# Kernel tuning notes

Measured on AMD Instinct MI355X. Metric: run time of the kernel, lower is better.

## Reference

```python
import jax, jax.numpy as jnp
import numpy as np

B, D, H, S = 65536, 256, 4, 64
HD = D // H  # head_dim = 64
EPS = 1e-8


def _lin(x, W, b):
    # torch nn.Linear: y = x @ W.T + b, W: [out, in]
    return x @ W.T + b


def _cos_attn(q_heads, keys, vals):
    # q_heads: [B,H,hd]; keys/vals: [H,S,hd] (shared across batch)
    qn = q_heads / (jnp.linalg.norm(q_heads, axis=-1, keepdims=True) + EPS)
    kn = keys / (jnp.linalg.norm(keys, axis=-1, keepdims=True) + EPS)
    sim = jnp.einsum('bhd,hsd->bhs', qn, kn)          # cosine sims, temp=1.0
    attn = jax.nn.softmax(sim, axis=-1)
    return jnp.einsum('bhs,hsd->bhd', attn, vals)     # [B,H,hd]


def setup_inputs() -> dict:
    key = jax.random.key(0)
    ks = jax.random.split(key, 20)

    def xavier(k, shape):
        fan_in, fan_out = shape[1], shape[0]
        lim = np.sqrt(6.0 / (fan_in + fan_out))
        return jax.random.uniform(k, shape, jnp.float32, -lim, lim)

    return {
        'query': jax.random.normal(ks[0], (B, D), jnp.float32),
        'context': jax.random.normal(ks[1], (B, D), jnp.float32),
        'fast_keys': 0.01 * jax.random.normal(ks[2], (H, S, HD), jnp.float32),
        'fast_vals': 0.01 * jax.random.normal(ks[3], (H, S, HD), jnp.float32),
        'deep_keys': 0.01 * jax.random.normal(ks[4], (H, S, HD), jnp.float32),
        'deep_vals': 0.01 * jax.random.normal(ks[5], (H, S, HD), jnp.float32),
        'Wq': xavier(ks[6], (D, D)), 'bq': jnp.zeros((D,), jnp.float32),
        'Wg': xavier(ks[7], (D, D)), 'bg': jnp.zeros((D,), jnp.float32),
        'Wc1': xavier(ks[8], (D // 2, D)), 'bc1': jnp.zeros((D // 2,), jnp.float32),
        'Wc2': xavier(ks[9], (1, D // 2)), 'bc2': jnp.zeros((1,), jnp.float32),
        'Wo': xavier(ks[10], (D, D)), 'bo': jnp.zeros((D,), jnp.float32),
        'Ws': xavier(ks[11], (D, D)), 'bs': jnp.zeros((D,), jnp.float32),
        'mix_logit': jnp.zeros((), jnp.float32),
        'surprise_mean': jnp.zeros((1, D), jnp.float32),
        'surprise_var': jnp.ones((1, D), jnp.float32),
    }


def reference(query, context, fast_keys, fast_vals, deep_keys, deep_vals,
              Wq, bq, Wg, bg, Wc1, bc1, Wc2, bc2, Wo, bo, Ws, bs,
              mix_logit, surprise_mean, surprise_var):
    # --- query projection and head split ---
    q = _lin(query, Wq, bq)                       # [B, D]
    q_heads = q.reshape(B, H, HD)                 # [B, H, hd]

    # --- dual-tier cosine-similarity attention reads ---
    v_fast = _cos_attn(q_heads, fast_keys, fast_vals).reshape(B, D)
    v_deep = _cos_attn(q_heads, deep_keys, deep_vals).reshape(B, D)

    # --- context-gated mixing of tiers ---
    gate = jnp.tanh(_lin(context, Wg, bg)).mean(axis=-1, keepdims=True)  # [B,1]
    mix = jax.nn.sigmoid(mix_logit + gate)
    out = mix * v_fast + (1.0 - mix) * v_deep

    # --- adaptive retrieval confidence head ---
    conf = jax.nn.sigmoid(_lin(jnp.tanh(_lin(context, Wc1, bc1)), Wc2, bc2))  # [B,1]
    out = out * conf
    out = _lin(out, Wo, bo)                       # [B, d_value]

    # --- surprise (detached diagnostic, does not feed output) ---
    h = jax.lax.stop_gradient(_lin(context, Ws, bs))
    z = (h - surprise_mean) / jnp.sqrt(surprise_var + 1e-6)
    surprise = jax.nn.sigmoid(jnp.abs(z).mean(axis=-1) - 2.0)  # 1/max(0.5,0.1)=2.0
    del surprise  # aux diagnostic; main output is the retrieved vector
    return out
```

## Files before the change

kernel.cpp:

```cpp
#include <hip/hip_runtime.h>

typedef unsigned short u16;
typedef __attribute__((ext_vector_type(8))) short bf16x8;
typedef __attribute__((ext_vector_type(4))) float f32x4;
typedef __attribute__((ext_vector_type(4))) unsigned short u16x4;

#define MFMA16(a, b, c) __builtin_amdgcn_mfma_f32_16x16x32_bf16((a), (b), (c), 0, 0, 0)

#define OFF_WQ   0
#define OFF_WG   65536
#define OFF_WC1  131072
#define OFF_WO   163840
#define OFF_KNF  229376
#define OFF_VTF  245760
#define OFF_KND  262144
#define OFF_VTD  278528

__device__ __forceinline__ u16 f2b(float f) {
  union { float f; unsigned u; } v; v.f = f;
  unsigned r = v.u + 0x7fffu + ((v.u >> 16) & 1u);
  return (u16)(r >> 16);
}
__device__ __forceinline__ float fsig(float x) {
  return __builtin_amdgcn_rcpf(1.f + __expf(-x));
}
__device__ __forceinline__ float ftanh(float x) {
  float e = __expf(2.f * x);
  return (e - 1.f) * __builtin_amdgcn_rcpf(e + 1.f);
}
__device__ __forceinline__ float sum16(float v) {
  v += __shfl_xor(v, 1);
  v += __shfl_xor(v, 2);
  v += __shfl_xor(v, 4);
  v += __shfl_xor(v, 8);
  return v;
}

__global__ void k_convert(const float* __restrict__ Wq, const float* __restrict__ Wg,
                          const float* __restrict__ Wc1, const float* __restrict__ Wo,
                          u16* __restrict__ ws) {
  int i = blockIdx.x * 256 + threadIdx.x;
  ws[OFF_WQ + i] = f2b(Wq[i]);
  ws[OFF_WG + i] = f2b(Wg[i]);
  ws[OFF_WO + i] = f2b(Wo[i]);
  if (i < 32768) ws[OFF_WC1 + i] = f2b(Wc1[i]);
}

__global__ void k_prep(const float* __restrict__ fk, const float* __restrict__ fv,
                       const float* __restrict__ dk, const float* __restrict__ dv,
                       u16* __restrict__ ws) {
  int t = blockIdx.x * 64 + threadIdx.x;
  int h = t >> 6, s = t & 63;
  const float* p;
  float ss, sc;

  p = fk + t * 64; ss = 0.f;
  for (int d = 0; d < 64; ++d) { float x = p[d]; ss += x * x; }
  sc = __builtin_amdgcn_rcpf(__builtin_amdgcn_sqrtf(ss) + 1e-8f);
  for (int d = 0; d < 64; ++d) ws[OFF_KNF + t * 64 + d] = f2b(p[d] * sc);

  p = dk + t * 64; ss = 0.f;
  for (int d = 0; d < 64; ++d) { float x = p[d]; ss += x * x; }
  sc = __builtin_amdgcn_rcpf(__builtin_amdgcn_sqrtf(ss) + 1e-8f);
  for (int d = 0; d < 64; ++d) ws[OFF_KND + t * 64 + d] = f2b(p[d] * sc);

  p = fv + t * 64;
  for (int d = 0; d < 64; ++d) ws[OFF_VTF + h * 4096 + d * 64 + s] = f2b(p[d]);
  p = dv + t * 64;
  for (int d = 0; d < 64; ++d) ws[OFF_VTD + h * 4096 + d * 64 + s] = f2b(p[d]);
}

__global__ __launch_bounds__(256, 2)
void k_fused(const float* __restrict__ query, const float* __restrict__ context,
             const float* __restrict__ bq, const float* __restrict__ bg,
             const float* __restrict__ bc1, const float* __restrict__ Wc2,
             const float* __restrict__ bc2v, const float* __restrict__ bo,
             const float* __restrict__ mixl, const u16* __restrict__ ws,
             float* __restrict__ outp) {
  __shared__ u16 sX[64 * 256];
  __shared__ float red_g[4][64];
  __shared__ float red_c[4][64];
  __shared__ float sA[64];
  __shared__ float sB[64];

  const int t = threadIdx.x;
  const int w = t >> 6;
  const int lane = t & 63;
  const int quad = lane >> 4;
  const int l16 = lane & 15;
  const int row4 = quad * 4;
  const int blk = blockIdx.x;
  char* Xb = (char*)sX;
  char* chunk = Xb + w * 8192;

  auto stage = [&](const float* src) {
    #pragma unroll
    for (int i = 0; i < 16; ++i) {
      int e = i * 1024 + t * 4;
      float4 v = *(const float4*)(src + e);
      int row = e >> 8, col = e & 255;
      u16x4 pk;
      pk.x = f2b(v.x); pk.y = f2b(v.y); pk.z = f2b(v.z); pk.w = f2b(v.w);
      *(u16x4*)(Xb + row * 512 + ((((col >> 3) ^ (row & 7)) << 4) | ((col & 7) << 1))) = pk;
    }
  };
  auto ldA = [&](int row, int kb) {
    return *(const bf16x8*)(Xb + row * 512 + ((((kb >> 3) ^ (row & 7)) << 4)));
  };
  auto ldC = [&](int row, int kb) {
    return *(const bf16x8*)(chunk + row * 128 + ((((kb >> 3) ^ (row & 7)) << 4)));
  };
  auto cwr = [&](int row, int col, u16 v) {
    *(u16*)(chunk + row * 128 + (((((col >> 3) ^ (row & 7)) << 3) | (col & 7)) << 1)) = v;
  };

  const f32x4 vzero = {0.f, 0.f, 0.f, 0.f};

  stage(context + (size_t)blk * 16384);
  __syncthreads();

  {
    f32x4 acc[4][4];
    #pragma unroll
    for (int mt = 0; mt < 4; ++mt)
      #pragma unroll
      for (int nt = 0; nt < 4; ++nt) acc[mt][nt] = vzero;
    const u16* WB = ws + OFF_WG + (w * 64 + l16) * 256;
    #pragma unroll
    for (int kk = 0; kk < 8; ++kk) {
      int kb = kk * 32 + quad * 8;
      bf16x8 a0 = ldA(l16, kb), a1 = ldA(16 + l16, kb), a2 = ldA(32 + l16, kb), a3 = ldA(48 + l16, kb);
      #pragma unroll
      for (int nt = 0; nt < 4; ++nt) {
        bf16x8 b = *(const bf16x8*)(WB + nt * 4096 + kb);
        acc[0][nt] = MFMA16(a0, b, acc[0][nt]);
        acc[1][nt] = MFMA16(a1, b, acc[1][nt]);
        acc[2][nt] = MFMA16(a2, b, acc[2][nt]);
        acc[3][nt] = MFMA16(a3, b, acc[3][nt]);
      }
    }
    float bgv[4];
    #pragma unroll
    for (int nt = 0; nt < 4; ++nt) bgv[nt] = bg[w * 64 + nt * 16 + l16];
    #pragma unroll
    for (int mt = 0; mt < 4; ++mt)
      #pragma unroll
      for (int r = 0; r < 4; ++r) {
        float s = 0.f;
        #pragma unroll
        for (int nt = 0; nt < 4; ++nt) s += ftanh(acc[mt][nt][r] + bgv[nt]);
        s = sum16(s);
        if (l16 == 0) red_g[w][mt * 16 + row4 + r] = s;
      }
  }
  {
    f32x4 acc[4][2];
    #pragma unroll
    for (int mt = 0; mt < 4; ++mt) { acc[mt][0] = vzero; acc[mt][1] = vzero; }
    const u16* WB = ws + OFF_WC1 + (w * 32 + l16) * 256;
    #pragma unroll
    for (int kk = 0; kk < 8; ++kk) {
      int kb = kk * 32 + quad * 8;
      bf16x8 a0 = ldA(l16, kb), a1 = ldA(16 + l16, kb), a2 = ldA(32 + l16, kb), a3 = ldA(48 + l16, kb);
      #pragma unroll
      for (int nt = 0; nt < 2; ++nt) {
        bf16x8 b = *(const bf16x8*)(WB + nt * 4096 + kb);
        acc[0][nt] = MFMA16(a0, b, acc[0][nt]);
        acc[1][nt] = MFMA16(a1, b, acc[1][nt]);
        acc[2][nt] = MFMA16(a2, b, acc[2][nt]);
        acc[3][nt] = MFMA16(a3, b, acc[3][nt]);
      }
    }
    float bcv[2], wcv[2];
    #pragma unroll
    for (int nt = 0; nt < 2; ++nt) {
      int n = w * 32 + nt * 16 + l16;
      bcv[nt] = bc1[n]; wcv[nt] = Wc2[n];
    }
    #pragma unroll
    for (int mt = 0; mt < 4; ++mt)
      #pragma unroll
      for (int r = 0; r < 4; ++r) {
        float s = 0.f;
        #pragma unroll
        for (int nt = 0; nt < 2; ++nt) s += ftanh(acc[mt][nt][r] + bcv[nt]) * wcv[nt];
        s = sum16(s);
        if (l16 == 0) red_c[w][mt * 16 + row4 + r] = s;
      }
  }
  __syncthreads();
  if (t < 64) {
    float g = (red_g[0][t] + red_g[1][t] + red_g[2][t] + red_g[3][t]) * (1.f / 256.f);
    float mix = fsig(mixl[0] + g);
    float conf = fsig(red_c[0][t] + red_c[1][t] + red_c[2][t] + red_c[3][t] + bc2v[0]);
    sA[t] = conf * mix;
    sB[t] = conf - conf * mix;
  }
  __syncthreads();

  stage(query + (size_t)blk * 16384);
  __syncthreads();

  f32x4 qa[4][4];
  {
    #pragma unroll
    for (int mt = 0; mt < 4; ++mt)
      #pragma unroll
      for (int nt = 0; nt < 4; ++nt) qa[mt][nt] = vzero;
    const u16* WB = ws + OFF_WQ + (w * 64 + l16) * 256;
    #pragma unroll
    for (int kk = 0; kk < 8; ++kk) {
      int kb = kk * 32 + quad * 8;
      bf16x8 a0 = ldA(l16, kb), a1 = ldA(16 + l16, kb), a2 = ldA(32 + l16, kb), a3 = ldA(48 + l16, kb);
      #pragma unroll
      for (int nt = 0; nt < 4; ++nt) {
        bf16x8 b = *(const bf16x8*)(WB + nt * 4096 + kb);
        qa[0][nt] = MFMA16(a0, b, qa[0][nt]);
        qa[1][nt] = MFMA16(a1, b, qa[1][nt]);
        qa[2][nt] = MFMA16(a2, b, qa[2][nt]);
        qa[3][nt] = MFMA16(a3, b, qa[3][nt]);
      }
    }
    float bqv[4];
    #pragma unroll
    for (int nt = 0; nt < 4; ++nt) bqv[nt] = bq[w * 64 + nt * 16 + l16];
    #pragma unroll
    for (int mt = 0; mt < 4; ++mt)
      #pragma unroll
      for (int nt = 0; nt < 4; ++nt)
        #pragma unroll
        for (int r = 0; r < 4; ++r) qa[mt][nt][r] += bqv[nt];
  }
  float scl[4][4];
  #pragma unroll
  for (int mt = 0; mt < 4; ++mt)
    #pragma unroll
    for (int r = 0; r < 4; ++r) {
      float ss = 0.f;
      #pragma unroll
      for (int nt = 0; nt < 4; ++nt) ss += qa[mt][nt][r] * qa[mt][nt][r];
      ss = sum16(ss);
      scl[mt][r] = __builtin_amdgcn_rcpf(__builtin_amdgcn_sqrtf(ss) + 1e-8f);
    }
  __syncthreads();

  #pragma unroll
  for (int mt = 0; mt < 4; ++mt)
    #pragma unroll
    for (int r = 0; r < 4; ++r) {
      int row = mt * 16 + row4 + r;
      #pragma unroll
      for (int nt = 0; nt < 4; ++nt)
        cwr(row, nt * 16 + l16, f2b(qa[mt][nt][r] * scl[mt][r]));
    }

  f32x4 sf[4][4], sd[4][4];
  #pragma unroll
  for (int mt = 0; mt < 4; ++mt)
    #pragma unroll
    for (int nt = 0; nt < 4; ++nt) { sf[mt][nt] = vzero; sd[mt][nt] = vzero; }
  {
    const u16* knF = ws + OFF_KNF + w * 4096;
    const u16* knD = ws + OFF_KND + w * 4096;
    #pragma unroll
    for (int kk = 0; kk < 2; ++kk) {
      int kb = kk * 32 + quad * 8;
      bf16x8 a0 = ldC(l16, kb), a1 = ldC(16 + l16, kb), a2 = ldC(32 + l16, kb), a3 = ldC(48 + l16, kb);
      #pragma unroll
      for (int nt = 0; nt < 4; ++nt) {
        bf16x8 bF = *(const bf16x8*)(knF + (nt * 16 + l16) * 64 + kb);
        bf16x8 bD = *(const bf16x8*)(knD + (nt * 16 + l16) * 64 + kb);
        sf[0][nt] = MFMA16(a0, bF, sf[0][nt]);
        sf[1][nt] = MFMA16(a1, bF, sf[1][nt]);
        sf[2][nt] = MFMA16(a2, bF, sf[2][nt]);
        sf[3][nt] = MFMA16(a3, bF, sf[3][nt]);
        sd[0][nt] = MFMA16(a0, bD, sd[0][nt]);
        sd[1][nt] = MFMA16(a1, bD, sd[1][nt]);
        sd[2][nt] = MFMA16(a2, bD, sd[2][nt]);
        sd[3][nt] = MFMA16(a3, bD, sd[3][nt]);
      }
    }
  }

  f32x4 oacc[4][4];
  {
    #pragma unroll
    for (int mt = 0; mt < 4; ++mt)
      #pragma unroll
      for (int r = 0; r < 4; ++r) {
        float rs = 0.f;
        #pragma unroll
        for (int nt = 0; nt < 4; ++nt) { float e = __expf(sf[mt][nt][r]); sf[mt][nt][r] = e; rs += e; }
        rs = sum16(rs);
        float inv = __builtin_amdgcn_rcpf(rs);
        int row = mt * 16 + row4 + r;
        #pragma unroll
        for (int nt = 0; nt < 4; ++nt) cwr(row, nt * 16 + l16, f2b(sf[mt][nt][r] * inv));
      }
    f32x4 pv[4][4];
    #pragma unroll
    for (int mt = 0; mt < 4; ++mt)
      #pragma unroll
      for (int nt = 0; nt < 4; ++nt) pv[mt][nt] = vzero;
    const u16* vT = ws + OFF_VTF + w * 4096;
    #pragma unroll
    for (int kk = 0; kk < 2; ++kk) {
      int kb = kk * 32 + quad * 8;
      bf16x8 a0 = ldC(l16, kb), a1 = ldC(16 + l16, kb), a2 = ldC(32 + l16, kb), a3 = ldC(48 + l16, kb);
      #pragma unroll
      for (int nt = 0; nt < 4; ++nt) {
        bf16x8 b = *(const bf16x8*)(vT + (nt * 16 + l16) * 64 + kb);
        pv[0][nt] = MFMA16(a0, b, pv[0][nt]);
        pv[1][nt] = MFMA16(a1, b, pv[1][nt]);
        pv[2][nt] = MFMA16(a2, b, pv[2][nt]);
        pv[3][nt] = MFMA16(a3, b, pv[3][nt]);
      }
    }
    #pragma unroll
    for (int mt = 0; mt < 4; ++mt)
      #pragma unroll
      for (int r = 0; r < 4; ++r) {
        float m_ = sA[mt * 16 + row4 + r];
        #pragma unroll
        for (int nt = 0; nt < 4; ++nt) oacc[mt][nt][r] = m_ * pv[mt][nt][r];
      }
  }
  {
    #pragma unroll
    for (int mt = 0; mt < 4; ++mt)
      #pragma unroll
      for (int r = 0; r < 4; ++r) {
        float rs = 0.f;
        #pragma unroll
        for (int nt = 0; nt < 4; ++nt) { float e = __expf(sd[mt][nt][r]); sd[mt][nt][r] = e; rs += e; }
        rs = sum16(rs);
        float inv = __builtin_amdgcn_rcpf(rs);
        int row = mt * 16 + row4 + r;
        #pragma unroll
        for (int nt = 0; nt < 4; ++nt) cwr(row, nt * 16 + l16, f2b(sd[mt][nt][r] * inv));
      }
    f32x4 pv[4][4];
    #pragma unroll
    for (int mt = 0; mt < 4; ++mt)
      #pragma unroll
      for (int nt = 0; nt < 4; ++nt) pv[mt][nt] = vzero;
    const u16* vT = ws + OFF_VTD + w * 4096;
    #pragma unroll
    for (int kk = 0; kk < 2; ++kk) {
      int kb = kk * 32 + quad * 8;
      bf16x8 a0 = ldC(l16, kb), a1 = ldC(16 + l16, kb), a2 = ldC(32 + l16, kb), a3 = ldC(48 + l16, kb);
      #pragma unroll
      for (int nt = 0; nt < 4; ++nt) {
        bf16x8 b = *(const bf16x8*)(vT + (nt * 16 + l16) * 64 + kb);
        pv[0][nt] = MFMA16(a0, b, pv[0][nt]);
        pv[1][nt] = MFMA16(a1, b, pv[1][nt]);
        pv[2][nt] = MFMA16(a2, b, pv[2][nt]);
        pv[3][nt] = MFMA16(a3, b, pv[3][nt]);
      }
    }
    #pragma unroll
    for (int mt = 0; mt < 4; ++mt)
      #pragma unroll
      for (int r = 0; r < 4; ++r) {
        float m_ = sB[mt * 16 + row4 + r];
        #pragma unroll
        for (int nt = 0; nt < 4; ++nt) oacc[mt][nt][r] += m_ * pv[mt][nt][r];
      }
  }

  __syncthreads();
  #pragma unroll
  for (int mt = 0; mt < 4; ++mt)
    #pragma unroll
    for (int r = 0; r < 4; ++r) {
      int row = mt * 16 + row4 + r;
      #pragma unroll
      for (int nt = 0; nt < 4; ++nt) {
        int col = w * 64 + nt * 16 + l16;
        *(u16*)(Xb + row * 512 + (((((col >> 3) ^ (row & 7)) << 3) | (col & 7)) << 1)) =
            f2b(oacc[mt][nt][r]);
      }
    }
  __syncthreads();

  {
    f32x4 o[4][4];
    #pragma unroll
    for (int mt = 0; mt < 4; ++mt)
      #pragma unroll
      for (int nt = 0; nt < 4; ++nt) o[mt][nt] = vzero;
    const u16* WB = ws + OFF_WO + (w * 64 + l16) * 256;
    #pragma unroll
    for (int kk = 0; kk < 8; ++kk) {
      int kb = kk * 32 + quad * 8;
      bf16x8 a0 = ldA(l16, kb), a1 = ldA(16 + l16, kb), a2 = ldA(32 + l16, kb), a3 = ldA(48 + l16, kb);
      #pragma unroll
      for (int nt = 0; nt < 4; ++nt) {
        bf16x8 b = *(const bf16x8*)(WB + nt * 4096 + kb);
        o[0][nt] = MFMA16(a0, b, o[0][nt]);
        o[1][nt] = MFMA16(a1, b, o[1][nt]);
        o[2][nt] = MFMA16(a2, b, o[2][nt]);
        o[3][nt] = MFMA16(a3, b, o[3][nt]);
      }
    }
    float bov[4];
    #pragma unroll
    for (int nt = 0; nt < 4; ++nt) bov[nt] = bo[w * 64 + nt * 16 + l16];
    float* dst = outp + (size_t)blk * 16384;
    #pragma unroll
    for (int mt = 0; mt < 4; ++mt)
      #pragma unroll
      for (int r = 0; r < 4; ++r) {
        int row = mt * 16 + row4 + r;
        #pragma unroll
        for (int nt = 0; nt < 4; ++nt)
          dst[row * 256 + w * 64 + nt * 16 + l16] = o[mt][nt][r] + bov[nt];
      }
  }
}

extern "C" void kernel_launch(void* const* d_in, const int* in_sizes, int n_in,
                              void* d_out, int out_size, void* d_ws, size_t ws_size,
                              hipStream_t stream) {
  const float* query   = (const float*)d_in[0];
  const float* context = (const float*)d_in[1];
  const float* fk      = (const float*)d_in[2];
  const float* fv      = (const float*)d_in[3];
  const float* dk      = (const float*)d_in[4];
  const float* dv      = (const float*)d_in[5];
  const float* Wq      = (const float*)d_in[6];
  const float* bq      = (const float*)d_in[7];
  const float* Wg      = (const float*)d_in[8];
  const float* bg      = (const float*)d_in[9];
  const float* Wc1     = (const float*)d_in[10];
  const float* bc1     = (const float*)d_in[11];
  const float* Wc2     = (const float*)d_in[12];
  const float* bc2     = (const float*)d_in[13];
  const float* Wo      = (const float*)d_in[14];
  const float* bo      = (const float*)d_in[15];
  const float* mixl    = (const float*)d_in[18];
  u16* ws = (u16*)d_ws;
  float* outp = (float*)d_out;

  k_convert<<<256, 256, 0, stream>>>(Wq, Wg, Wc1, Wo, ws);
  k_prep<<<4, 64, 0, stream>>>(fk, fv, dk, dv, ws);
  k_fused<<<1024, 256, 0, stream>>>(query, context, bq, bg, bc1, Wc2, bc2, bo,
                                    mixl, ws, outp);
}
```

Measured before the change: 326.8 us.

## Use 512-thread blocks with fragment-ordered weights and merged prep kernel

Doubles threads per block to 8 waves, so each wave handles half the output columns and the attention work is split per head and per half of the rows. Weights and normalized keys/values are pre-permuted into MFMA fragment order so each lane does a single contiguous 16-byte load. The gate and confidence GEMMs are fused into one K loop. The two prep kernels are merged into one launch. This raises occupancy and latency hiding, at the cost of an extra cross-wave reduction for the query norm, more barriers, and higher register pressure under launch_bounds(512,4).

Result: faster. 295.4 us (-9.6%).

```diff
diff --git a/kernel.cpp b/kernel.cpp
--- a/kernel.cpp
+++ b/kernel.cpp
@@ -4,6 +4,7 @@
 typedef __attribute__((ext_vector_type(8))) short bf16x8;
 typedef __attribute__((ext_vector_type(4))) float f32x4;
 typedef __attribute__((ext_vector_type(4))) unsigned short u16x4;
+typedef __attribute__((ext_vector_type(8))) unsigned short u16x8;
 
 #define MFMA16(a, b, c) __builtin_amdgcn_mfma_f32_16x16x32_bf16((a), (b), (c), 0, 0, 0)
 
@@ -36,41 +37,61 @@
   return v;
 }
 
-__global__ void k_convert(const float* __restrict__ Wq, const float* __restrict__ Wg,
-                          const float* __restrict__ Wc1, const float* __restrict__ Wo,
-                          u16* __restrict__ ws) {
-  int i = blockIdx.x * 256 + threadIdx.x;
-  ws[OFF_WQ + i] = f2b(Wq[i]);
-  ws[OFF_WG + i] = f2b(Wg[i]);
-  ws[OFF_WO + i] = f2b(Wo[i]);
-  if (i < 32768) ws[OFF_WC1 + i] = f2b(Wc1[i]);
-}
-
-__global__ void k_prep(const float* __restrict__ fk, const float* __restrict__ fv,
+__global__ void k_prep(const float* __restrict__ Wq, const float* __restrict__ Wg,
+                       const float* __restrict__ Wc1, const float* __restrict__ Wo,
+                       const float* __restrict__ fk, const float* __restrict__ fv,
                        const float* __restrict__ dk, const float* __restrict__ dv,
                        u16* __restrict__ ws) {
-  int t = blockIdx.x * 64 + threadIdx.x;
-  int h = t >> 6, s = t & 63;
-  const float* p;
-  float ss, sc;
-
-  p = fk + t * 64; ss = 0.f;
-  for (int d = 0; d < 64; ++d) { float x = p[d]; ss += x * x; }
-  sc = __builtin_amdgcn_rcpf(__builtin_amdgcn_sqrtf(ss) + 1e-8f);
-  for (int d = 0; d < 64; ++d) ws[OFF_KNF + t * 64 + d] = f2b(p[d] * sc);
-
-  p = dk + t * 64; ss = 0.f;
-  for (int d = 0; d < 64; ++d) { float x = p[d]; ss += x * x; }
-  sc = __builtin_amdgcn_rcpf(__builtin_amdgcn_sqrtf(ss) + 1e-8f);
-  for (int d = 0; d < 64; ++d) ws[OFF_KND + t * 64 + d] = f2b(p[d] * sc);
-
-  p = fv + t * 64;
-  for (int d = 0; d < 64; ++d) ws[OFF_VTF + h * 4096 + d * 64 + s] = f2b(p[d]);
-  p = dv + t * 64;
-  for (int d = 0; d < 64; ++d) ws[OFF_VTD + h * 4096 + d * 64 + s] = f2b(p[d]);
-}
-
-__global__ __launch_bounds__(256, 2)
+  const int bid = blockIdx.x, t = threadIdx.x;
+  if (bid < 96) {
+    const float* W = bid < 32 ? Wq : (bid < 64 ? Wg : Wo);
+    const int OFF = bid < 32 ? OFF_WQ : (bid < 64 ? OFF_WG : OFF_WO);
+    int c = (bid & 31) * 256 + t;
+    int lane = c & 63, nt = (c >> 6) & 1, kk = (c >> 7) & 7, w = c >> 10;
+    const float* s = W + (w * 32 + nt * 16 + (lane & 15)) * 256 + kk * 32 + ((lane >> 4) & 3) * 8;
+    u16x8 o;
+    #pragma unroll
+    for (int j = 0; j < 8; ++j) o[j] = f2b(s[j]);
+    *(u16x8*)(ws + OFF + c * 8) = o;
+  } else if (bid < 112) {
+    int c = (bid - 96) * 256 + t;
+    int lane = c & 63, kk = (c >> 6) & 7, w = c >> 9;
+    const float* s = Wc1 + (w * 16 + (lane & 15)) * 256 + kk * 32 + ((lane >> 4) & 3) * 8;
+    u16x8 o;
+    #pragma unroll
+    for (int j = 0; j < 8; ++j) o[j] = f2b(s[j]);
+    *(u16x8*)(ws + OFF_WC1 + c * 8) = o;
+  } else {
+    int idx = (bid - 112) * 256 + t;
+    int st = idx >> 8, rowid = idx & 255;
+    int h = rowid >> 6, s = rowid & 63;
+    if (st < 2) {
+      const float* p = (st == 0 ? fk : dk) + rowid * 64;
+      const int OFF = (st == 0) ? OFF_KNF : OFF_KND;
+      float ss = 0.f;
+      #pragma unroll
+      for (int d = 0; d < 64; ++d) { float x = p[d]; ss += x * x; }
+      float sc = __builtin_amdgcn_rcpf(__builtin_amdgcn_sqrtf(ss) + 1e-8f);
+      int nt = s >> 4, sl = s & 15;
+      #pragma unroll
+      for (int d = 0; d < 64; ++d) {
+        int lane = ((d >> 3) & 3) * 16 + sl;
+        ws[OFF + (((h * 2 + (d >> 5)) * 4 + nt) * 64 + lane) * 8 + (d & 7)] = f2b(p[d] * sc);
+      }
+    } else {
+      const float* p = (st == 2 ? fv : dv) + rowid * 64;
+      const int OFF = (st == 2) ? OFF_VTF : OFF_VTD;
+      int kk = s >> 5, quad = (s >> 3) & 3, j = s & 7;
+      #pragma unroll
+      for (int d = 0; d < 64; ++d) {
+        int lane = quad * 16 + (d & 15);
+        ws[OFF + (((h * 2 + kk) * 4 + (d >> 4)) * 64 + lane) * 8 + j] = f2b(p[d]);
+      }
+    }
+  }
+}
+
+__global__ __launch_bounds__(512, 4)
 void k_fused(const float* __restrict__ query, const float* __restrict__ context,
              const float* __restrict__ bq, const float* __restrict__ bg,
              const float* __restrict__ bc1, const float* __restrict__ Wc2,
@@ -78,8 +99,8 @@
              const float* __restrict__ mixl, const u16* __restrict__ ws,
              float* __restrict__ outp) {
   __shared__ u16 sX[64 * 256];
-  __shared__ float red_g[4][64];
-  __shared__ float red_c[4][64];
+  __shared__ float red_a[8][64];
+  __shared__ float red_c[8][64];
   __shared__ float sA[64];
   __shared__ float sB[64];
 
@@ -89,14 +110,16 @@
   const int quad = lane >> 4;
   const int l16 = lane & 15;
   const int row4 = quad * 4;
+  const int h = w >> 1;
+  const int rh = (w & 1) * 32;
   const int blk = blockIdx.x;
   char* Xb = (char*)sX;
-  char* chunk = Xb + w * 8192;
+  char* Ch = Xb + h * 8192;
 
   auto stage = [&](const float* src) {
     #pragma unroll
-    for (int i = 0; i < 16; ++i) {
-      int e = i * 1024 + t * 4;
+    for (int i = 0; i < 8; ++i) {
+      int e = i * 2048 + t * 4;
       float4 v = *(const float4*)(src + e);
       int row = e >> 8, col = e & 255;
       u16x4 pk;
@@ -108,140 +131,104 @@
     return *(const bf16x8*)(Xb + row * 512 + ((((kb >> 3) ^ (row & 7)) << 4)));
   };
   auto ldC = [&](int row, int kb) {
-    return *(const bf16x8*)(chunk + row * 128 + ((((kb >> 3) ^ (row & 7)) << 4)));
+    return *(const bf16x8*)(Ch + row * 128 + ((((kb >> 3) ^ (row & 7)) << 4)));
   };
   auto cwr = [&](int row, int col, u16 v) {
-    *(u16*)(chunk + row * 128 + (((((col >> 3) ^ (row & 7)) << 3) | (col & 7)) << 1)) = v;
+    *(u16*)(Ch + row * 128 + (((((col >> 3) ^ (row & 7)) << 3) | (col & 7)) << 1)) = v;
   };
 
   const f32x4 vzero = {0.f, 0.f, 0.f, 0.f};
 
   stage(context + (size_t)blk * 16384);
+  float bgv[2], bqv[2], bov[2];
+  #pragma unroll
+  for (int nt = 0; nt < 2; ++nt) {
+    int n = w * 32 + nt * 16 + l16;
+    bgv[nt] = bg[n]; bqv[nt] = bq[n]; bov[nt] = bo[n];
+  }
+  float bc1v = bc1[w * 16 + l16];
+  float wc2v = Wc2[w * 16 + l16];
   __syncthreads();
 
   {
-    f32x4 acc[4][4];
-    #pragma unroll
-    for (int mt = 0; mt < 4; ++mt)
-      #pragma unroll
-      for (int nt = 0; nt < 4; ++nt) acc[mt][nt] = vzero;
-    const u16* WB = ws + OFF_WG + (w * 64 + l16) * 256;
+    f32x4 ag[4][2], ac[4];
+    #pragma unroll
+    for (int mt = 0; mt < 4; ++mt) { ag[mt][0] = vzero; ag[mt][1] = vzero; ac[mt] = vzero; }
     #pragma unroll
     for (int kk = 0; kk < 8; ++kk) {
       int kb = kk * 32 + quad * 8;
       bf16x8 a0 = ldA(l16, kb), a1 = ldA(16 + l16, kb), a2 = ldA(32 + l16, kb), a3 = ldA(48 + l16, kb);
       #pragma unroll
-      for (int nt = 0; nt < 4; ++nt) {
-        bf16x8 b = *(const bf16x8*)(WB + nt * 4096 + kb);
-        acc[0][nt] = MFMA16(a0, b, acc[0][nt]);
-        acc[1][nt] = MFMA16(a1, b, acc[1][nt]);
-        acc[2][nt] = MFMA16(a2, b, acc[2][nt]);
-        acc[3][nt] = MFMA16(a3, b, acc[3][nt]);
-      }
-    }
-    float bgv[4];
-    #pragma unroll
-    for (int nt = 0; nt < 4; ++nt) bgv[nt] = bg[w * 64 + nt * 16 + l16];
+      for (int nt = 0; nt < 2; ++nt) {
+        bf16x8 b = *(const bf16x8*)(ws + OFF_WG + (((w * 8 + kk) * 2 + nt) * 64 + lane) * 8);
+        ag[0][nt] = MFMA16(a0, b, ag[0][nt]);
+        ag[1][nt] = MFMA16(a1, b, ag[1][nt]);
+        ag[2][nt] = MFMA16(a2, b, ag[2][nt]);
+        ag[3][nt] = MFMA16(a3, b, ag[3][nt]);
+      }
+      bf16x8 bc = *(const bf16x8*)(ws + OFF_WC1 + ((w * 8 + kk) * 64 + lane) * 8);
+      ac[0] = MFMA16(a0, bc, ac[0]);
+      ac[1] = MFMA16(a1, bc, ac[1]);
+      ac[2] = MFMA16(a2, bc, ac[2]);
+      ac[3] = MFMA16(a3, bc, ac[3]);
+    }
     #pragma unroll
     for (int mt = 0; mt < 4; ++mt)
       #pragma unroll
       for (int r = 0; r < 4; ++r) {
-        float s = 0.f;
-        #pragma unroll
-        for (int nt = 0; nt < 4; ++nt) s += ftanh(acc[mt][nt][r] + bgv[nt]);
-        s = sum16(s);
-        if (l16 == 0) red_g[w][mt * 16 + row4 + r] = s;
-      }
-  }
+        float sg = ftanh(ag[mt][0][r] + bgv[0]) + ftanh(ag[mt][1][r] + bgv[1]);
+        sg = sum16(sg);
+        float sc = ftanh(ac[mt][r] + bc1v) * wc2v;
+        sc = sum16(sc);
+        if (l16 == 0) { red_a[w][mt * 16 + row4 + r] = sg; red_c[w][mt * 16 + row4 + r] = sc; }
+      }
+  }
+  __syncthreads();
+
+  if (t < 64) {
+    float g = 0.f, cc = 0.f;
+    #pragma unroll
+    for (int i = 0; i < 8; ++i) { g += red_a[i][t]; cc += red_c[i][t]; }
+    float mix = fsig(mixl[0] + g * (1.f / 256.f));
+    float conf = fsig(cc + bc2v[0]);
+    sA[t] = conf * mix;
+    sB[t] = conf - conf * mix;
+  }
+  stage(query + (size_t)blk * 16384);
+  __syncthreads();
+
+  f32x4 qa[4][2];
   {
-    f32x4 acc[4][2];
-    #pragma unroll
-    for (int mt = 0; mt < 4; ++mt) { acc[mt][0] = vzero; acc[mt][1] = vzero; }
-    const u16* WB = ws + OFF_WC1 + (w * 32 + l16) * 256;
+    #pragma unroll
+    for (int mt = 0; mt < 4; ++mt) { qa[mt][0] = vzero; qa[mt][1] = vzero; }
     #pragma unroll
     for (int kk = 0; kk < 8; ++kk) {
       int kb = kk * 32 + quad * 8;
       bf16x8 a0 = ldA(l16, kb), a1 = ldA(16 + l16, kb), a2 = ldA(32 + l16, kb), a3 = ldA(48 + l16, kb);
       #pragma unroll
       for (int nt = 0; nt < 2; ++nt) {
-        bf16x8 b = *(const bf16x8*)(WB + nt * 4096 + kb);
-        acc[0][nt] = MFMA16(a0, b, acc[0][nt]);
-        acc[1][nt] = MFMA16(a1, b, acc[1][nt]);
-        acc[2][nt] = MFMA16(a2, b, acc[2][nt]);
-        acc[3][nt] = MFMA16(a3, b, acc[3][nt]);
-      }
-    }
-    float bcv[2], wcv[2];
-    #pragma unroll
-    for (int nt = 0; nt < 2; ++nt) {
-      int n = w * 32 + nt * 16 + l16;
-      bcv[nt] = bc1[n]; wcv[nt] = Wc2[n];
-    }
-    #pragma unroll
-    for (int mt = 0; mt < 4; ++mt)
-      #pragma unroll
-      for (int r = 0; r < 4; ++r) {
-        float s = 0.f;
-        #pragma unroll
-        for (int nt = 0; nt < 2; ++nt) s += ftanh(acc[mt][nt][r] + bcv[nt]) * wcv[nt];
-        s = sum16(s);
-        if (l16 == 0) red_c[w][mt * 16 + row4 + r] = s;
-      }
-  }
-  __syncthreads();
-  if (t < 64) {
-    float g = (red_g[0][t] + red_g[1][t] + red_g[2][t] + red_g[3][t]) * (1.f / 256.f);
-    float mix = fsig(mixl[0] + g);
-    float conf = fsig(red_c[0][t] + red_c[1][t] + red_c[2][t] + red_c[3][t] + bc2v[0]);
-    sA[t] = conf * mix;
-    sB[t] = conf - conf * mix;
-  }
-  __syncthreads();
-
-  stage(query + (size_t)blk * 16384);
-  __syncthreads();
-
-  f32x4 qa[4][4];
-  {
-    #pragma unroll
-    for (int mt = 0; mt < 4; ++mt)
-      #pragma unroll
-      for (int nt = 0; nt < 4; ++nt) qa[mt][nt] = vzero;
-    const u16* WB = ws + OFF_WQ + (w * 64 + l16) * 256;
-    #pragma unroll
-    for (int kk = 0; kk < 8; ++kk) {
-      int kb = kk * 32 + quad * 8;
-      bf16x8 a0 = ldA(l16, kb), a1 = ldA(16 + l16, kb), a2 = ldA(32 + l16, kb), a3 = ldA(48 + l16, kb);
-      #pragma unroll
-      for (int nt = 0; nt < 4; ++nt) {
-        bf16x8 b = *(const bf16x8*)(WB + nt * 4096 + kb);
+        bf16x8 b = *(const bf16x8*)(ws + OFF_WQ + (((w * 8 + kk) * 2 + nt) * 64 + lane) * 8);
         qa[0][nt] = MFMA16(a0, b, qa[0][nt]);
         qa[1][nt] = MFMA16(a1, b, qa[1][nt]);
         qa[2][nt] = MFMA16(a2, b, qa[2][nt]);
         qa[3][nt] = MFMA16(a3, b, qa[3][nt]);
       }
     }
-    float bqv[4];
-    #pragma unroll
-    for (int nt = 0; nt < 4; ++nt) bqv[nt] = bq[w * 64 + nt * 16 + l16];
     #pragma unroll
     for (int mt = 0; mt < 4; ++mt)
       #pragma unroll
-      for (int nt = 0; nt < 4; ++nt)
-        #pragma unroll
-        for (int r = 0; r < 4; ++r) qa[mt][nt][r] += bqv[nt];
-  }
-  float scl[4][4];
-  #pragma unroll
-  for (int mt = 0; mt < 4; ++mt)
-    #pragma unroll
-    for (int r = 0; r < 4; ++r) {
-      float ss = 0.f;
-      #pragma unroll
-      for (int nt = 0; nt < 4; ++nt) ss += qa[mt][nt][r] * qa[mt][nt][r];
-      ss = sum16(ss);
-      scl[mt][r] = __builtin_amdgcn_rcpf(__builtin_amdgcn_sqrtf(ss) + 1e-8f);
-    }
+      for (int r = 0; r < 4; ++r) {
+        float ss = 0.f;
+        #pragma unroll
+        for (int nt = 0; nt < 2; ++nt) {
+          float q_ = qa[mt][nt][r] + bqv[nt];
+          qa[mt][nt][r] = q_;
+          ss += q_ * q_;
+        }
+        ss = sum16(ss);
+        if (l16 == 0) red_a[w][mt * 16 + row4 + r] = ss;
+      }
+  }
   __syncthreads();
 
   #pragma unroll
@@ -249,43 +236,42 @@
     #pragma unroll
     for (int r = 0; r < 4; ++r) {
       int row = mt * 16 + row4 + r;
-      #pragma unroll
-      for (int nt = 0; nt < 4; ++nt)
-        cwr(row, nt * 16 + l16, f2b(qa[mt][nt][r] * scl[mt][r]));
-    }
-
-  f32x4 sf[4][4], sd[4][4];
-  #pragma unroll
-  for (int mt = 0; mt < 4; ++mt)
+      float ss = red_a[w][row] + red_a[w ^ 1][row];
+      float scl = __builtin_amdgcn_rcpf(__builtin_amdgcn_sqrtf(ss) + 1e-8f);
+      #pragma unroll
+      for (int nt = 0; nt < 2; ++nt)
+        cwr(row, (w & 1) * 32 + nt * 16 + l16, f2b(qa[mt][nt][r] * scl));
+    }
+  __syncthreads();
+
+  bf16x8 qf[2][2];
+  #pragma unroll
+  for (int mt = 0; mt < 2; ++mt)
+    #pragma unroll
+    for (int kk = 0; kk < 2; ++kk)
+      qf[mt][kk] = ldC(rh + mt * 16 + l16, kk * 32 + quad * 8);
+
+  f32x4 sf[2][4], sd[2][4];
+  #pragma unroll
+  for (int mt = 0; mt < 2; ++mt)
     #pragma unroll
     for (int nt = 0; nt < 4; ++nt) { sf[mt][nt] = vzero; sd[mt][nt] = vzero; }
+  #pragma unroll
+  for (int kk = 0; kk < 2; ++kk)
+    #pragma unroll
+    for (int nt = 0; nt < 4; ++nt) {
+      bf16x8 bF = *(const bf16x8*)(ws + OFF_KNF + (((h * 2 + kk) * 4 + nt) * 64 + lane) * 8);
+      bf16x8 bD = *(const bf16x8*)(ws + OFF_KND + (((h * 2 + kk) * 4 + nt) * 64 + lane) * 8);
+      sf[0][nt] = MFMA16(qf[0][kk], bF, sf[0][nt]);
+      sf[1][nt] = MFMA16(qf[1][kk], bF, sf[1][nt]);
+      sd[0][nt] = MFMA16(qf[0][kk], bD, sd[0][nt]);
+      sd[1][nt] = MFMA16(qf[1][kk], bD, sd[1][nt]);
+    }
+
+  f32x4 oacc[2][4];
   {
-    const u16* knF = ws + OFF_KNF + w * 4096;
-    const u16* knD = ws + OFF_KND + w * 4096;
-    #pragma unroll
-    for (int kk = 0; kk < 2; ++kk) {
-      int kb = kk * 32 + quad * 8;
-      bf16x8 a0 = ldC(l16, kb), a1 = ldC(16 + l16, kb), a2 = ldC(32 + l16, kb), a3 = ldC(48 + l16, kb);
-      #pragma unroll
-      for (int nt = 0; nt < 4; ++nt) {
-        bf16x8 bF = *(const bf16x8*)(knF + (nt * 16 + l16) * 64 + kb);
-        bf16x8 bD = *(const bf16x8*)(knD + (nt * 16 + l16) * 64 + kb);
-        sf[0][nt] = MFMA16(a0, bF, sf[0][nt]);
-        sf[1][nt] = MFMA16(a1, bF, sf[1][nt]);
-        sf[2][nt] = MFMA16(a2, bF, sf[2][nt]);
-        sf[3][nt] = MFMA16(a3, bF, sf[3][nt]);
-        sd[0][nt] = MFMA16(a0, bD, sd[0][nt]);
-        sd[1][nt] = MFMA16(a1, bD, sd[1][nt]);
-        sd[2][nt] = MFMA16(a2, bD, sd[2][nt]);
-        sd[3][nt] = MFMA16(a3, bD, sd[3][nt]);
-      }
-    }
-  }
-
-  f32x4 oacc[4][4];
-  {
-    #pragma unroll
-    for (int mt = 0; mt < 4; ++mt)
+    #pragma unroll
+    for (int mt = 0; mt < 2; ++mt)
       #pragma unroll
       for (int r = 0; r < 4; ++r) {
         float rs = 0.f;
@@ -293,41 +279,37 @@
         for (int nt = 0; nt < 4; ++nt) { float e = __expf(sf[mt][nt][r]); sf[mt][nt][r] = e; rs += e; }
         rs = sum16(rs);
         float inv = __builtin_amdgcn_rcpf(rs);
-        int row = mt * 16 + row4 + r;
+        int row = rh + mt * 16 + row4 + r;
         #pragma unroll
         for (int nt = 0; nt < 4; ++nt) cwr(row, nt * 16 + l16, f2b(sf[mt][nt][r] * inv));
       }
-    f32x4 pv[4][4];
-    #pragma unroll
-    for (int mt = 0; mt < 4; ++mt)
+    bf16x8 pf00 = ldC(rh + l16, quad * 8),      pf01 = ldC(rh + l16, 32 + quad * 8);
+    bf16x8 pf10 = ldC(rh + 16 + l16, quad * 8), pf11 = ldC(rh + 16 + l16, 32 + quad * 8);
+    f32x4 pv[2][4];
+    #pragma unroll
+    for (int mt = 0; mt < 2; ++mt)
       #pragma unroll
       for (int nt = 0; nt < 4; ++nt) pv[mt][nt] = vzero;
-    const u16* vT = ws + OFF_VTF + w * 4096;
-    #pragma unroll
-    for (int kk = 0; kk < 2; ++kk) {
-      int kb = kk * 32 + quad * 8;
-      bf16x8 a0 = ldC(l16, kb), a1 = ldC(16 + l16, kb), a2 = ldC(32 + l16, kb), a3 = ldC(48 + l16, kb);
+    #pragma unroll
+    for (int kk = 0; kk < 2; ++kk)
       #pragma unroll
       for (int nt = 0; nt < 4; ++nt) {
-        bf16x8 b = *(const bf16x8*)(vT + (nt * 16 + l16) * 64 + kb);
-        pv[0][nt] = MFMA16(a0, b, pv[0][nt]);
-        pv[1][nt] = MFMA16(a1, b, pv[1][nt]);
-        pv[2][nt] = MFMA16(a2, b, pv[2][nt]);
-        pv[3][nt] = MFMA16(a3, b, pv[3][nt]);
-      }
-    }
-    #pragma unroll
-    for (int mt = 0; mt < 4; ++mt)
-      #pragma unroll
-      for (int r = 0; r < 4; ++r) {
-        float m_ = sA[mt * 16 + row4 + r];
+        bf16x8 b = *(const bf16x8*)(ws + OFF_VTF + (((h * 2 + kk) * 4 + nt) * 64 + lane) * 8);
+        pv[0][nt] = MFMA16(kk ? pf01 : pf00, b, pv[0][nt]);
+        pv[1][nt] = MFMA16(kk ? pf11 : pf10, b, pv[1][nt]);
+      }
+    #pragma unroll
+    for (int mt = 0; mt < 2; ++mt)
+      #pragma unroll
+      for (int r = 0; r < 4; ++r) {
+        float m_ = sA[rh + mt * 16 + row4 + r];
         #pragma unroll
         for (int nt = 0; nt < 4; ++nt) oacc[mt][nt][r] = m_ * pv[mt][nt][r];
       }
   }
   {
     #pragma unroll
-    for (int mt = 0; mt < 4; ++mt)
+    for (int mt = 0; mt < 2; ++mt)
       #pragma unroll
       for (int r = 0; r < 4; ++r) {
         float rs = 0.f;
@@ -335,34 +317,30 @@
         for (int nt = 0; nt < 4; ++nt) { float e = __expf(sd[mt][nt][r]); sd[mt][nt][r] = e; rs += e; }
         rs = sum16(rs);
         float inv = __builtin_amdgcn_rcpf(rs);
-        int row = mt * 16 + row4 + r;
+        int row = rh + mt * 16 + row4 + r;
         #pragma unroll
         for (int nt = 0; nt < 4; ++nt) cwr(row, nt * 16 + l16, f2b(sd[mt][nt][r] * inv));
       }
-    f32x4 pv[4][4];
-    #pragma unroll
-    for (int mt = 0; mt < 4; ++mt)
+    bf16x8 pf00 = ldC(rh + l16, quad * 8),      pf01 = ldC(rh + l16, 32 + quad * 8);
+    bf16x8 pf10 = ldC(rh + 16 + l16, quad * 8), pf11 = ldC(rh + 16 + l16, 32 + quad * 8);
+    f32x4 pv[2][4];
+    #pragma unroll
+    for (int mt = 0; mt < 2; ++mt)
       #pragma unroll
       for (int nt = 0; nt < 4; ++nt) pv[mt][nt] = vzero;
-    const u16* vT = ws + OFF_VTD + w * 4096;
-    #pragma unroll
-    for (int kk = 0; kk < 2; ++kk) {
-      int kb = kk * 32 + quad * 8;
-      bf16x8 a0 = ldC(l16, kb), a1 = ldC(16 + l16, kb), a2 = ldC(32 + l16, kb), a3 = ldC(48 + l16, kb);
+    #pragma unroll
+    for (int kk = 0; kk < 2; ++kk)
       #pragma unroll
       for (int nt = 0; nt < 4; ++nt) {
-        bf16x8 b = *(const bf16x8*)(vT + (nt * 16 + l16) * 64 + kb);
-        pv[0][nt] = MFMA16(a0, b, pv[0][nt]);
-        pv[1][nt] = MFMA16(a1, b, pv[1][nt]);
-        pv[2][nt] = MFMA16(a2, b, pv[2][nt]);
-        pv[3][nt] = MFMA16(a3, b, pv[3][nt]);
-      }
-    }
-    #pragma unroll
-    for (int mt = 0; mt < 4; ++mt)
-      #pragma unroll
-      for (int r = 0; r < 4; ++r) {
-        float m_ = sB[mt * 16 + row4 + r];
+        bf16x8 b = *(const bf16x8*)(ws + OFF_VTD + (((h * 2 + kk) * 4 + nt) * 64 + lane) * 8);
+        pv[0][nt] = MFMA16(kk ? pf01 : pf00, b, pv[0][nt]);
+        pv[1][nt] = MFMA16(kk ? pf11 : pf10, b, pv[1][nt]);
+      }
+    #pragma unroll
+    for (int mt = 0; mt < 2; ++mt)
+      #pragma unroll
+      for (int r = 0; r < 4; ++r) {
+        float m_ = sB[rh + mt * 16 + row4 + r];
         #pragma unroll
         for (int nt = 0; nt < 4; ++nt) oacc[mt][nt][r] += m_ * pv[mt][nt][r];
       }
@@ -370,42 +348,36 @@
 
   __syncthreads();
   #pragma unroll
-  for (int mt = 0; mt < 4; ++mt)
+  for (int mt = 0; mt < 2; ++mt)
     #pragma unroll
     for (int r = 0; r < 4; ++r) {
-      int row = mt * 16 + row4 + r;
+      int row = rh + mt * 16 + row4 + r;
       #pragma unroll
       for (int nt = 0; nt < 4; ++nt) {
-        int col = w * 64 + nt * 16 + l16;
-        *(u16*)(Xb + row * 512 + (((((col >> 3) ^ (row & 7)) << 3) | (col & 7)) << 1)) =
+        int col = h * 64 + nt * 16 + l16;
+        *(u16*)(Xb + row * 512 + ((((col >> 3) ^ (row & 7)) << 4) | ((col & 7) << 1))) =
             f2b(oacc[mt][nt][r]);
       }
     }
   __syncthreads();
 
   {
-    f32x4 o[4][4];
-    #pragma unroll
-    for (int mt = 0; mt < 4; ++mt)
-      #pragma unroll
-      for (int nt = 0; nt < 4; ++nt) o[mt][nt] = vzero;
-    const u16* WB = ws + OFF_WO + (w * 64 + l16) * 256;
+    f32x4 o[4][2];
+    #pragma unroll
+    for (int mt = 0; mt < 4; ++mt) { o[mt][0] = vzero; o[mt][1] = vzero; }
     #pragma unroll
     for (int kk = 0; kk < 8; ++kk) {
       int kb = kk * 32 + quad * 8;
       bf16x8 a0 = ldA(l16, kb), a1 = ldA(16 + l16, kb), a2 = ldA(32 + l16, kb), a3 = ldA(48 + l16, kb);
       #pragma unroll
-      for (int nt = 0; nt < 4; ++nt) {
-        bf16x8 b = *(const bf16x8*)(WB + nt * 4096 + kb);
+      for (int nt = 0; nt < 2; ++nt) {
+        bf16x8 b = *(const bf16x8*)(ws + OFF_WO + (((w * 8 + kk) * 2 + nt) * 64 + lane) * 8);
         o[0][nt] = MFMA16(a0, b, o[0][nt]);
         o[1][nt] = MFMA16(a1, b, o[1][nt]);
         o[2][nt] = MFMA16(a2, b, o[2][nt]);
         o[3][nt] = MFMA16(a3, b, o[3][nt]);
       }
     }
-    float bov[4];
-    #pragma unroll
-    for (int nt = 0; nt < 4; ++nt) bov[nt] = bo[w * 64 + nt * 16 + l16];
     float* dst = outp + (size_t)blk * 16384;
     #pragma unroll
     for (int mt = 0; mt < 4; ++mt)
@@ -413,8 +385,8 @@
       for (int r = 0; r < 4; ++r) {
         int row = mt * 16 + row4 + r;
         #pragma unroll
-        for (int nt = 0; nt < 4; ++nt)
-          dst[row * 256 + w * 64 + nt * 16 + l16] = o[mt][nt][r] + bov[nt];
+        for (int nt = 0; nt < 2; ++nt)
+          dst[row * 256 + w * 32 + nt * 16 + l16] = o[mt][nt][r] + bov[nt];
       }
   }
 }
@@ -442,8 +414,7 @@
   u16* ws = (u16*)d_ws;
   float* outp = (float*)d_out;
 
-  k_convert<<<256, 256, 0, stream>>>(Wq, Wg, Wc1, Wo, ws);
-  k_prep<<<4, 64, 0, stream>>>(fk, fv, dk, dv, ws);
-  k_fused<<<1024, 256, 0, stream>>>(query, context, bq, bg, bc1, Wc2, bc2, bo,
+  k_prep<<<116, 256, 0, stream>>>(Wq, Wg, Wc1, Wo, fk, fv, dk, dv, ws);
+  k_fused<<<1024, 512, 0, stream>>>(query, context, bq, bg, bc1, Wc2, bc2, bo,
                                     mixl, ws, outp);
 }
```
